# Performance work log

Hardware: AMD Instinct MI355X
Metric: run time of the kernel (lower is better)

The kernel has to match this reference:

```python
import jax, jax.numpy as jnp
import numpy as np

N, D, E, L = 50000, 128, 800000, 3


def setup_inputs() -> dict:
    key = jax.random.key(0)
    ks = jax.random.split(key, 4)
    scale = 1.0 / np.sqrt(D)
    x = jax.random.normal(ks[0], (N, D), dtype=jnp.float32)
    edge_index = jax.random.randint(ks[1], (2, E), 0, N, dtype=jnp.int64)
    W1 = jax.random.normal(ks[2], (L, D, D), dtype=jnp.float32) * scale
    W2 = jax.random.normal(ks[3], (L, D, D), dtype=jnp.float32) * scale
    b1 = jnp.zeros((L, D), dtype=jnp.float32)
    b2 = jnp.zeros((L, D), dtype=jnp.float32)
    return {"x": x, "edge_index": edge_index, "W1": W1, "b1": b1, "W2": W2, "b2": b2}


def reference(x, edge_index, W1, b1, W2, b2):
    # GIN: for each conv, agg_i = (1+eps)*x_i + sum_{(j->i)} x_j  (eps=0),
    # then h = nn(agg) with nn = Linear->ReLU->Linear, then outer ReLU.
    src = edge_index[0]
    dst = edge_index[1]
    n = x.shape[0]
    for l in range(W1.shape[0]):
        agg = x + jax.ops.segment_sum(x[src], dst, num_segments=n)  # [N, D]
        h = jnp.maximum(agg @ W1[l] + b1[l], 0.0)                   # inner ReLU
        x = jnp.maximum(h @ W2[l] + b2[l], 0.0)                     # outer ReLU
    return x
```

## Files before the change

### kernel.cpp

```cpp
#include <hip/hip_runtime.h>
#include <cstdint>


constexpr int N = 50000;
constexpr int D = 128;
constexpr int E = 800000;
constexpr int L = 3;
constexpr int NB_SCAN = (N + 255) / 256;
constexpr int WROW = 136;

typedef _Float16 f16;
typedef _Float16 f16x8 __attribute__((ext_vector_type(8)));
typedef float f32x4 __attribute__((ext_vector_type(4)));

__device__ __forceinline__ bool ei_is64(const int* ei) {
  return (ei[1] == 0) && (ei[3] == 0) && (ei[5] == 0);
}
__device__ __forceinline__ int ei_src(const int* ei, int e, bool is64) {
  return is64 ? ei[2 * (size_t)e] : ei[e];
}
__device__ __forceinline__ int ei_dst(const int* ei, int e, bool is64) {
  return is64 ? ei[2 * ((size_t)E + e)] : ei[(size_t)E + e];
}

__global__ __launch_bounds__(256) void k_init(const float* __restrict__ x0,
                                              const int* __restrict__ ei,
                                              const float* __restrict__ W1,
                                              const float* __restrict__ W2,
                                              f16* __restrict__ Wt,
                                              f16* __restrict__ xh,
                                              int* __restrict__ dst32,
                                              int2* __restrict__ srk,
                                              int* __restrict__ cnt) {
  const int bid = blockIdx.x;
  if (bid < 384) {
    int i = bid * 256 + threadIdx.x;
    int m = i >> 14;
    int c = (i >> 7) & 127;
    int k = i & 127;
    const float* src = (m < L) ? (W1 + (size_t)m * D * D)
                               : (W2 + (size_t)(m - L) * D * D);
    Wt[i] = (f16)src[(size_t)k * D + c];
  } else if (bid < 384 + 3125) {
    int i = (bid - 384) * 256 + threadIdx.x;
    float4 v0 = *(const float4*)(x0 + (size_t)i * 8);
    float4 v1 = *(const float4*)(x0 + (size_t)i * 8 + 4);
    f16x8 o = {(f16)v0.x, (f16)v0.y, (f16)v0.z, (f16)v0.w,
               (f16)v1.x, (f16)v1.y, (f16)v1.z, (f16)v1.w};
    *(f16x8*)(xh + (size_t)i * 8) = o;
  } else {
    int e = (bid - (384 + 3125)) * 256 + threadIdx.x;
    bool is64 = ei_is64(ei);
    int s = ei_src(ei, e, is64);
    int t = ei_dst(ei, e, is64);
    dst32[e] = t;
    int r = atomicAdd(cnt + t, 1);
    srk[e] = make_int2(s, r);
  }
}

__global__ __launch_bounds__(256) void k_scan1(const int* __restrict__ cnt,
                                               int* __restrict__ off,
                                               int* __restrict__ bsum) {
  __shared__ int s[256];
  int i = blockIdx.x * 256 + threadIdx.x;
  int v = (i < N) ? cnt[i] : 0;
  s[threadIdx.x] = v;
  __syncthreads();
#pragma unroll
  for (int o = 1; o < 256; o <<= 1) {
    int t = (threadIdx.x >= o) ? s[threadIdx.x - o] : 0;
    __syncthreads();
    s[threadIdx.x] += t;
    __syncthreads();
  }
  if (i < N) off[i] = s[threadIdx.x] - v;
  if (threadIdx.x == 255) bsum[blockIdx.x] = s[255];
}

__global__ __launch_bounds__(256) void k_scan2(int* __restrict__ bsum) {
  __shared__ int s[256];
  int v = (threadIdx.x < NB_SCAN) ? bsum[threadIdx.x] : 0;
  s[threadIdx.x] = v;
  __syncthreads();
#pragma unroll
  for (int o = 1; o < 256; o <<= 1) {
    int t = (threadIdx.x >= o) ? s[threadIdx.x - o] : 0;
    __syncthreads();
    s[threadIdx.x] += t;
    __syncthreads();
  }
  if (threadIdx.x < NB_SCAN) bsum[threadIdx.x] = s[threadIdx.x] - v;
}

__global__ __launch_bounds__(256) void k_scan3(int* __restrict__ off,
                                               const int* __restrict__ bsum) {
  int i = blockIdx.x * 256 + threadIdx.x;
  if (i < N) off[i] += bsum[i >> 8];
  if (i == 0) off[N] = E;
}

__global__ __launch_bounds__(256) void k_bucket(const int* __restrict__ dst32,
                                                const int2* __restrict__ srk,
                                                const int* __restrict__ off,
                                                int* __restrict__ ssrc) {
  int e = blockIdx.x * 256 + threadIdx.x;
  int d = dst32[e];
  int2 sr = srk[e];
  ssrc[off[d] + sr.y] = sr.x;
}

__global__ __launch_bounds__(256) void k_gather_f16(const f16* __restrict__ x,
                                                    const int* __restrict__ off,
                                                    const int* __restrict__ ssrc,
                                                    f16* __restrict__ agg) {
  int n = blockIdx.x * 16 + (threadIdx.x >> 4);
  if (n >= N) return;
  const int d0 = (threadIdx.x & 15) << 3;
  f16x8 v = *(const f16x8*)(x + (size_t)n * D + d0);
  float acc[8];
#pragma unroll
  for (int j = 0; j < 8; ++j) acc[j] = (float)v[j];
  const int beg = off[n], end = off[n + 1];
  int p = beg;
  for (; p + 8 <= end; p += 8) {
    f16x8 u[8];
#pragma unroll
    for (int q = 0; q < 8; ++q) {
      int s = ssrc[p + q];
      u[q] = *(const f16x8*)(x + (size_t)s * D + d0);
    }
#pragma unroll
    for (int q = 0; q < 8; ++q)
#pragma unroll
      for (int j = 0; j < 8; ++j) acc[j] += (float)u[q][j];
  }
  if (p + 4 <= end) {
    f16x8 u[4];
#pragma unroll
    for (int q = 0; q < 4; ++q) {
      int s = ssrc[p + q];
      u[q] = *(const f16x8*)(x + (size_t)s * D + d0);
    }
#pragma unroll
    for (int q = 0; q < 4; ++q)
#pragma unroll
      for (int j = 0; j < 8; ++j) acc[j] += (float)u[q][j];
    p += 4;
  }
  for (; p < end; ++p) {
    int s = ssrc[p];
    f16x8 u = *(const f16x8*)(x + (size_t)s * D + d0);
#pragma unroll
    for (int j = 0; j < 8; ++j) acc[j] += (float)u[j];
  }
  f16x8 o;
#pragma unroll
  for (int j = 0; j < 8; ++j) o[j] = (f16)acc[j];
  *(f16x8*)(agg + (size_t)n * D + d0) = o;
}

__global__ __launch_bounds__(256) void k_gemm_fused(const f16* __restrict__ A,
                                                    const f16* __restrict__ Wt1,
                                                    const f16* __restrict__ Wt2,
                                                    const float* __restrict__ b1,
                                                    const float* __restrict__ b2,
                                                    f16* __restrict__ Ch,
                                                    float* __restrict__ Cf) {
  __shared__ f16 Ws[2][128 * WROW];
  {
    const f16x8* g1 = (const f16x8*)Wt1;
    const f16x8* g2 = (const f16x8*)Wt2;
    for (int i = threadIdx.x; i < 2048; i += 256) {
      int c = i >> 4;
      int k8 = (i & 15) << 3;
      *(f16x8*)&Ws[0][c * WROW + k8] = g1[i];
      *(f16x8*)&Ws[1][c * WROW + k8] = g2[i];
    }
  }
  __syncthreads();

  const int w = threadIdx.x >> 6;
  const int l = threadIdx.x & 63;
  const int l15 = l & 15;
  const int g = l >> 4;
  const int r0 = blockIdx.x * 64 + w * 16;

  const int arow = min(r0 + l15, N - 1);
  const f16* Arow = A + (size_t)arow * D;
  f16x8 a[4];
#pragma unroll
  for (int t = 0; t < 4; ++t)
    a[t] = *(const f16x8*)(Arow + t * 32 + g * 8);

  float bc1[8], bc2[8];
#pragma unroll
  for (int c = 0; c < 8; ++c) {
    bc1[c] = b1[c * 16 + l15];
    bc2[c] = b2[c * 16 + l15];
  }

  f32x4 acc[8];
#pragma unroll
  for (int c = 0; c < 8; ++c) acc[c] = (f32x4){0.f, 0.f, 0.f, 0.f};
#pragma unroll
  for (int t = 0; t < 4; ++t) {
#pragma unroll
    for (int c = 0; c < 8; ++c) {
      f16x8 b = *(const f16x8*)&Ws[0][(c * 16 + l15) * WROW + t * 32 + g * 8];
      acc[c] = __builtin_amdgcn_mfma_f32_16x16x32_f16(a[t], b, acc[c], 0, 0, 0);
    }
  }

  __syncthreads();

  f16* hbuf = &Ws[0][0];
#pragma unroll
  for (int r = 0; r < 4; ++r) {
    int hr = w * 16 + g * 4 + r;
#pragma unroll
    for (int c = 0; c < 8; ++c) {
      float vv = fmaxf(acc[c][r] + bc1[c], 0.0f);
      hbuf[hr * WROW + c * 16 + l15] = (f16)vv;
    }
  }
  __syncthreads();

  f16x8 a2[4];
#pragma unroll
  for (int t = 0; t < 4; ++t)
    a2[t] = *(const f16x8*)&hbuf[(w * 16 + l15) * WROW + t * 32 + g * 8];

#pragma unroll
  for (int c = 0; c < 8; ++c) acc[c] = (f32x4){0.f, 0.f, 0.f, 0.f};
#pragma unroll
  for (int t = 0; t < 4; ++t) {
#pragma unroll
    for (int c = 0; c < 8; ++c) {
      f16x8 b = *(const f16x8*)&Ws[1][(c * 16 + l15) * WROW + t * 32 + g * 8];
      acc[c] = __builtin_amdgcn_mfma_f32_16x16x32_f16(a2[t], b, acc[c], 0, 0, 0);
    }
  }

#pragma unroll
  for (int r = 0; r < 4; ++r) {
    int rr = r0 + g * 4 + r;
    if (rr < N) {
#pragma unroll
      for (int c = 0; c < 8; ++c) {
        int col = c * 16 + l15;
        float vv = fmaxf(acc[c][r] + bc2[c], 0.0f);
        Ch[(size_t)rr * D + col] = (f16)vv;
        if (Cf) Cf[(size_t)rr * D + col] = vv;
      }
    }
  }
}

extern "C" void kernel_launch(void* const* d_in, const int* in_sizes, int n_in,
                              void* d_out, int out_size, void* d_ws, size_t ws_size,
                              hipStream_t stream) {
  const float* x0 = (const float*)d_in[0];
  const int* ei   = (const int*)d_in[1];
  const float* W1 = (const float*)d_in[2];
  const float* b1 = (const float*)d_in[3];
  const float* W2 = (const float*)d_in[4];
  const float* b2 = (const float*)d_in[5];
  float* out = (float*)d_out;

  f16* xh    = (f16*)d_ws;
  f16* aggh  = xh + (size_t)N * D;
  f16* Wt    = aggh + (size_t)N * D;
  int2* srk  = (int2*)(Wt + (size_t)2 * L * D * D);
  int* dst32 = (int*)(srk + E);
  int* off   = dst32 + E;
  int* cnt   = off + (N + 1);
  int* bsum  = cnt + N;
  int* ssrc  = bsum + 256;

  const dim3 blk(256);

  hipMemsetAsync(cnt, 0, (size_t)N * sizeof(int), stream);
  k_init<<<384 + 3125 + 3125, blk, 0, stream>>>(x0, ei, W1, W2, Wt, xh, dst32,
                                                srk, cnt);
  k_scan1<<<NB_SCAN, blk, 0, stream>>>(cnt, off, bsum);
  k_scan2<<<1, blk, 0, stream>>>(bsum);
  k_scan3<<<NB_SCAN, blk, 0, stream>>>(off, bsum);
  k_bucket<<<E / 256, blk, 0, stream>>>(dst32, srk, off, ssrc);

  const int gemm_blocks = (N + 63) / 64;
  const int gather_blocks = N / 16;

  for (int l = 0; l < L; ++l) {
    k_gather_f16<<<gather_blocks, blk, 0, stream>>>(xh, off, ssrc, aggh);
    k_gemm_fused<<<gemm_blocks, blk, 0, stream>>>(
        aggh, Wt + (size_t)l * D * D, Wt + (size_t)(L + l) * D * D,
        b1 + (size_t)l * D, b2 + (size_t)l * D, xh,
        (l == L - 1) ? out : nullptr);
  }
}
```

Before: 217.2 us.

## Privatize edge-count atomics per XCC to avoid cross-die contention

Replicates the per-destination edge counter eight times, one copy per XCC, and picks the copy from a hardware register read. The atomic increment uses workgroup scope with relaxed ordering, so it can stay in the local L2 instead of going through device-coherent memory. The scans merge the eight copies into one offset and write per-copy sub-offsets that the bucket kernel uses to scatter. This adds memset and scan traffic, and the correctness of the workgroup-scope atomics depends on each XCC having its own L2 and on the hardware register ID field being read correctly.

```diff
diff --git a/kernel.cpp b/kernel.cpp
--- a/kernel.cpp
+++ b/kernel.cpp
@@ -49,13 +49,15 @@
                (f16)v1.x, (f16)v1.y, (f16)v1.z, (f16)v1.w};
     *(f16x8*)(xh + (size_t)i * 8) = o;
   } else {
+    const int q = (int)(__builtin_amdgcn_s_getreg(6164)) & 7;
     int e = (bid - (384 + 3125)) * 256 + threadIdx.x;
     bool is64 = ei_is64(ei);
     int s = ei_src(ei, e, is64);
     int t = ei_dst(ei, e, is64);
     dst32[e] = t;
-    int r = atomicAdd(cnt + t, 1);
-    srk[e] = make_int2(s, r);
+    int r = __hip_atomic_fetch_add(cnt + (size_t)q * N + t, 1,
+                                   __ATOMIC_RELAXED, __HIP_MEMORY_SCOPE_WORKGROUP);
+    srk[e] = make_int2(s, r | (q << 29));
   }
 }
 
@@ -64,7 +66,11 @@
                                                int* __restrict__ bsum) {
   __shared__ int s[256];
   int i = blockIdx.x * 256 + threadIdx.x;
-  int v = (i < N) ? cnt[i] : 0;
+  int v = 0;
+  if (i < N) {
+#pragma unroll
+    for (int q = 0; q < 8; ++q) v += cnt[(size_t)q * N + i];
+  }
   s[threadIdx.x] = v;
   __syncthreads();
 #pragma unroll
@@ -94,20 +100,33 @@
 }
 
 __global__ __launch_bounds__(256) void k_scan3(int* __restrict__ off,
-                                               const int* __restrict__ bsum) {
+                                               const int* __restrict__ bsum,
+                                               const int* __restrict__ cnt,
+                                               int* __restrict__ offq) {
   int i = blockIdx.x * 256 + threadIdx.x;
-  if (i < N) off[i] += bsum[i >> 8];
+  if (i < N) {
+    int base = off[i] + bsum[i >> 8];
+    off[i] = base;
+    int run = base;
+#pragma unroll
+    for (int q = 0; q < 8; ++q) {
+      offq[(size_t)i * 8 + q] = run;
+      run += cnt[(size_t)q * N + i];
+    }
+  }
   if (i == 0) off[N] = E;
 }
 
 __global__ __launch_bounds__(256) void k_bucket(const int* __restrict__ dst32,
                                                 const int2* __restrict__ srk,
-                                                const int* __restrict__ off,
+                                                const int* __restrict__ offq,
                                                 int* __restrict__ ssrc) {
   int e = blockIdx.x * 256 + threadIdx.x;
   int d = dst32[e];
   int2 sr = srk[e];
-  ssrc[off[d] + sr.y] = sr.x;
+  int q = (int)((unsigned)sr.y >> 29);
+  int r = sr.y & 0x1FFFFFFF;
+  ssrc[offq[(size_t)d * 8 + q] + r] = sr.x;
 }
 
 __global__ __launch_bounds__(256) void k_gather_f16(const f16* __restrict__ x,
@@ -275,18 +294,19 @@
   int* dst32 = (int*)(srk + E);
   int* off   = dst32 + E;
   int* cnt   = off + (N + 1);
-  int* bsum  = cnt + N;
+  int* offq  = cnt + (size_t)8 * N;
+  int* bsum  = offq + (size_t)8 * N;
   int* ssrc  = bsum + 256;
 
   const dim3 blk(256);
 
-  hipMemsetAsync(cnt, 0, (size_t)N * sizeof(int), stream);
+  hipMemsetAsync(cnt, 0, (size_t)8 * N * sizeof(int), stream);
   k_init<<<384 + 3125 + 3125, blk, 0, stream>>>(x0, ei, W1, W2, Wt, xh, dst32,
                                                 srk, cnt);
   k_scan1<<<NB_SCAN, blk, 0, stream>>>(cnt, off, bsum);
   k_scan2<<<1, blk, 0, stream>>>(bsum);
-  k_scan3<<<NB_SCAN, blk, 0, stream>>>(off, bsum);
-  k_bucket<<<E / 256, blk, 0, stream>>>(dst32, srk, off, ssrc);
+  k_scan3<<<NB_SCAN, blk, 0, stream>>>(off, bsum, cnt, offq);
+  k_bucket<<<E / 256, blk, 0, stream>>>(dst32, srk, offq, ssrc);
 
   const int gemm_blocks = (N + 63) / 64;
   const int gather_blocks = N / 16;
```

Result: slower. 224.5 us (+3.3%).

## Replace global-atomic CSR build with two-level partitioned counting sort

Applied to the files above, without the earlier changes.

Replaces the per-edge global atomic counting, three-kernel scan and random bucket scatter with a two-pass radix-style sort. Edges are first binned by destination partition (512 nodes each) using shared-memory histograms, then each partition is sorted locally in shared memory to produce the offsets and the sorted source list. The aim is to remove contended global atomics and scattered writes, at the cost of an extra intermediate int2 buffer, more kernels and serial scan loops inside blocks. Within each destination, neighbour order may differ from before because shared atomics assign the ranks.

```diff
diff --git a/kernel.cpp b/kernel.cpp
--- a/kernel.cpp
+++ b/kernel.cpp
@@ -6,8 +6,12 @@
 constexpr int D = 128;
 constexpr int E = 800000;
 constexpr int L = 3;
-constexpr int NB_SCAN = (N + 255) / 256;
 constexpr int WROW = 136;
+constexpr int PSH = 9;
+constexpr int PN = 1 << PSH;
+constexpr int K = (N + PN - 1) >> PSH;
+constexpr int ABLK = 2048;
+constexpr int NAB = (E + ABLK - 1) / ABLK;
 
 typedef _Float16 f16;
 typedef _Float16 f16x8 __attribute__((ext_vector_type(8)));
@@ -29,9 +33,9 @@
                                               const float* __restrict__ W2,
                                               f16* __restrict__ Wt,
                                               f16* __restrict__ xh,
-                                              int* __restrict__ dst32,
-                                              int2* __restrict__ srk,
-                                              int* __restrict__ cnt) {
+                                              int2* __restrict__ srcdst,
+                                              int* __restrict__ gcnt) {
+  __shared__ int hist[K];
   const int bid = blockIdx.x;
   if (bid < 384) {
     int i = bid * 256 + threadIdx.x;
@@ -49,65 +53,145 @@
                (f16)v1.x, (f16)v1.y, (f16)v1.z, (f16)v1.w};
     *(f16x8*)(xh + (size_t)i * 8) = o;
   } else {
-    int e = (bid - (384 + 3125)) * 256 + threadIdx.x;
+    const int b = bid - (384 + 3125);
+    for (int i = threadIdx.x; i < K; i += 256) hist[i] = 0;
+    __syncthreads();
+    const int base = b * ABLK;
+    const int nHere = min(ABLK, E - base);
     bool is64 = ei_is64(ei);
-    int s = ei_src(ei, e, is64);
-    int t = ei_dst(ei, e, is64);
-    dst32[e] = t;
-    int r = atomicAdd(cnt + t, 1);
-    srk[e] = make_int2(s, r);
-  }
-}
-
-__global__ __launch_bounds__(256) void k_scan1(const int* __restrict__ cnt,
-                                               int* __restrict__ off,
-                                               int* __restrict__ bsum) {
+#pragma unroll
+    for (int r = 0; r < ABLK / 256; ++r) {
+      int idx = r * 256 + threadIdx.x;
+      if (idx < nHere) {
+        int e = base + idx;
+        int s = ei_src(ei, e, is64);
+        int d = ei_dst(ei, e, is64);
+        srcdst[e] = make_int2(s, d);
+        atomicAdd(&hist[d >> PSH], 1);
+      }
+    }
+    __syncthreads();
+    for (int i = threadIdx.x; i < K; i += 256) gcnt[i * NAB + b] = hist[i];
+  }
+}
+
+__global__ __launch_bounds__(256) void k_gbase(const int* __restrict__ gcnt,
+                                               int* __restrict__ gbase,
+                                               int* __restrict__ psize) {
   __shared__ int s[256];
-  int i = blockIdx.x * 256 + threadIdx.x;
-  int v = (i < N) ? cnt[i] : 0;
-  s[threadIdx.x] = v;
+  __shared__ int carry;
+  const int p = blockIdx.x;
+  const int tid = threadIdx.x;
+  if (tid == 0) carry = 0;
+  __syncthreads();
+  for (int chunk = 0; chunk < 2; ++chunk) {
+    int i = chunk * 256 + tid;
+    int v = (i < NAB) ? gcnt[p * NAB + i] : 0;
+    s[tid] = v;
+    __syncthreads();
+#pragma unroll
+    for (int o = 1; o < 256; o <<= 1) {
+      int t = (tid >= o) ? s[tid - o] : 0;
+      __syncthreads();
+      s[tid] += t;
+      __syncthreads();
+    }
+    int excl = s[tid] - v + carry;
+    if (i < NAB) gbase[p * NAB + i] = excl;
+    __syncthreads();
+    if (tid == 255) carry = carry + s[255];
+    __syncthreads();
+  }
+  if (tid == 0) psize[p] = carry;
+}
+
+__global__ __launch_bounds__(256) void k_pscan(const int* __restrict__ psize,
+                                               int* __restrict__ pbase,
+                                               int* __restrict__ off) {
+  __shared__ int s[256];
+  const int tid = threadIdx.x;
+  int v = (tid < K) ? psize[tid] : 0;
+  s[tid] = v;
   __syncthreads();
 #pragma unroll
   for (int o = 1; o < 256; o <<= 1) {
-    int t = (threadIdx.x >= o) ? s[threadIdx.x - o] : 0;
-    __syncthreads();
-    s[threadIdx.x] += t;
-    __syncthreads();
-  }
-  if (i < N) off[i] = s[threadIdx.x] - v;
-  if (threadIdx.x == 255) bsum[blockIdx.x] = s[255];
-}
-
-__global__ __launch_bounds__(256) void k_scan2(int* __restrict__ bsum) {
+    int t = (tid >= o) ? s[tid - o] : 0;
+    __syncthreads();
+    s[tid] += t;
+    __syncthreads();
+  }
+  if (tid < K) pbase[tid] = s[tid] - v;
+  if (tid == 0) { pbase[K] = E; off[N] = E; }
+}
+
+__global__ __launch_bounds__(256) void k_scat(const int2* __restrict__ srcdst,
+                                              const int* __restrict__ gbase,
+                                              const int* __restrict__ pbase,
+                                              int2* __restrict__ part) {
+  __shared__ int rankc[K];
+  const int b = blockIdx.x;
+  const int tid = threadIdx.x;
+  for (int i = tid; i < K; i += 256) rankc[i] = 0;
+  __syncthreads();
+  const int base = b * ABLK;
+  const int nHere = min(ABLK, E - base);
+#pragma unroll
+  for (int r = 0; r < ABLK / 256; ++r) {
+    int idx = r * 256 + tid;
+    if (idx < nHere) {
+      int2 sd = srcdst[base + idx];
+      int p = sd.y >> PSH;
+      int lr = atomicAdd(&rankc[p], 1);
+      part[pbase[p] + gbase[p * NAB + b] + lr] = sd;
+    }
+  }
+}
+
+__global__ __launch_bounds__(256) void k_fin(const int2* __restrict__ part,
+                                             const int* __restrict__ pbase,
+                                             int* __restrict__ off,
+                                             int* __restrict__ ssrc) {
+  __shared__ int hist[PN];
+  __shared__ int bbase[PN];
+  __shared__ int rc[PN];
   __shared__ int s[256];
-  int v = (threadIdx.x < NB_SCAN) ? bsum[threadIdx.x] : 0;
-  s[threadIdx.x] = v;
-  __syncthreads();
-#pragma unroll
-  for (int o = 1; o < 256; o <<= 1) {
-    int t = (threadIdx.x >= o) ? s[threadIdx.x - o] : 0;
-    __syncthreads();
-    s[threadIdx.x] += t;
-    __syncthreads();
-  }
-  if (threadIdx.x < NB_SCAN) bsum[threadIdx.x] = s[threadIdx.x] - v;
-}
-
-__global__ __launch_bounds__(256) void k_scan3(int* __restrict__ off,
-                                               const int* __restrict__ bsum) {
-  int i = blockIdx.x * 256 + threadIdx.x;
-  if (i < N) off[i] += bsum[i >> 8];
-  if (i == 0) off[N] = E;
-}
-
-__global__ __launch_bounds__(256) void k_bucket(const int* __restrict__ dst32,
-                                                const int2* __restrict__ srk,
-                                                const int* __restrict__ off,
-                                                int* __restrict__ ssrc) {
-  int e = blockIdx.x * 256 + threadIdx.x;
-  int d = dst32[e];
-  int2 sr = srk[e];
-  ssrc[off[d] + sr.y] = sr.x;
+  __shared__ int carry;
+  const int p = blockIdx.x;
+  const int tid = threadIdx.x;
+  const int lo = p << PSH;
+  const int nn = min(PN, N - lo);
+  const int ebeg = pbase[p], eend = pbase[p + 1];
+  for (int i = tid; i < PN; i += 256) { hist[i] = 0; rc[i] = 0; }
+  if (tid == 0) carry = 0;
+  __syncthreads();
+  for (int e = ebeg + tid; e < eend; e += 256)
+    atomicAdd(&hist[part[e].y - lo], 1);
+  __syncthreads();
+  for (int chunk = 0; chunk < PN / 256; ++chunk) {
+    int i = chunk * 256 + tid;
+    int v = hist[i];
+    s[tid] = v;
+    __syncthreads();
+#pragma unroll
+    for (int o = 1; o < 256; o <<= 1) {
+      int t = (tid >= o) ? s[tid - o] : 0;
+      __syncthreads();
+      s[tid] += t;
+      __syncthreads();
+    }
+    bbase[i] = s[tid] - v + carry;
+    __syncthreads();
+    if (tid == 255) carry = carry + s[255];
+    __syncthreads();
+  }
+  for (int i = tid; i < nn; i += 256) off[lo + i] = ebeg + bbase[i];
+  __syncthreads();
+  for (int e = ebeg + tid; e < eend; e += 256) {
+    int2 sd = part[e];
+    int b = sd.y - lo;
+    int r = atomicAdd(&rc[b], 1);
+    ssrc[ebeg + bbase[b] + r] = sd.x;
+  }
 }
 
 __global__ __launch_bounds__(256) void k_gather_f16(const f16* __restrict__ x,
@@ -268,25 +352,26 @@
   const float* b2 = (const float*)d_in[5];
   float* out = (float*)d_out;
 
-  f16* xh    = (f16*)d_ws;
-  f16* aggh  = xh + (size_t)N * D;
-  f16* Wt    = aggh + (size_t)N * D;
-  int2* srk  = (int2*)(Wt + (size_t)2 * L * D * D);
-  int* dst32 = (int*)(srk + E);
-  int* off   = dst32 + E;
-  int* cnt   = off + (N + 1);
-  int* bsum  = cnt + N;
-  int* ssrc  = bsum + 256;
+  f16* xh      = (f16*)d_ws;
+  f16* aggh    = xh + (size_t)N * D;
+  f16* Wt      = aggh + (size_t)N * D;
+  int2* srcdst = (int2*)(Wt + (size_t)2 * L * D * D);
+  int2* part   = srcdst + E;
+  int* gcnt    = (int*)(part + E);
+  int* gbase   = gcnt + (size_t)K * NAB;
+  int* psize   = gbase + (size_t)K * NAB;
+  int* pbase   = psize + K;
+  int* off     = pbase + (K + 1);
+  int* ssrc    = off + (N + 1);
 
   const dim3 blk(256);
 
-  hipMemsetAsync(cnt, 0, (size_t)N * sizeof(int), stream);
-  k_init<<<384 + 3125 + 3125, blk, 0, stream>>>(x0, ei, W1, W2, Wt, xh, dst32,
-                                                srk, cnt);
-  k_scan1<<<NB_SCAN, blk, 0, stream>>>(cnt, off, bsum);
-  k_scan2<<<1, blk, 0, stream>>>(bsum);
-  k_scan3<<<NB_SCAN, blk, 0, stream>>>(off, bsum);
-  k_bucket<<<E / 256, blk, 0, stream>>>(dst32, srk, off, ssrc);
+  k_init<<<384 + 3125 + NAB, blk, 0, stream>>>(x0, ei, W1, W2, Wt, xh, srcdst,
+                                               gcnt);
+  k_gbase<<<K, blk, 0, stream>>>(gcnt, gbase, psize);
+  k_pscan<<<1, blk, 0, stream>>>(psize, pbase, off);
+  k_scat<<<NAB, blk, 0, stream>>>(srcdst, gbase, pbase, part);
+  k_fin<<<K, blk, 0, stream>>>(part, pbase, off, ssrc);
 
   const int gemm_blocks = (N + 63) / 64;
   const int gather_blocks = N / 16;
```

Result: faster. 193.4 us (-10.9%).
